# Kernel tuning notes

Hardware: AMD Instinct MI355X
Metric: run time of the kernel (lower is better)

Reference implementation:

```python
import jax, jax.numpy as jnp
import numpy as np

N, L, D = 4, 2048, 1024
H_DIM, OUT_DIM = 1024, 1024


def setup_inputs() -> dict:
    key = jax.random.key(0)
    ks = jax.random.split(key, 7)
    scale = 0.02
    return {
        "x": jax.random.normal(ks[0], (N, L, D), dtype=jnp.float32),
        "Wq": jax.random.normal(ks[1], (D, H_DIM), dtype=jnp.float32) * scale,
        "bq": jnp.zeros((H_DIM,), dtype=jnp.float32),
        "Wk": jax.random.normal(ks[2], (D, H_DIM), dtype=jnp.float32) * scale,
        "bk": jnp.zeros((H_DIM,), dtype=jnp.float32),
        "Wv": jax.random.normal(ks[3], (D, OUT_DIM), dtype=jnp.float32) * scale,
        "bv": jnp.zeros((OUT_DIM,), dtype=jnp.float32),
    }


def reference(x, Wq, bq, Wk, bk, Wv, bv):
    # q,k: [N,L,h_dim], v: [N,L,out_dim]
    q = jnp.einsum("nld,dh->nlh", x, Wq) + bq
    k = jnp.einsum("nld,dh->nlh", x, Wk) + bk
    v = jnp.einsum("nld,do->nlo", x, Wv) + bv
    # scores: [N,L,L]
    qk = jnp.einsum("nlh,nmh->nlm", q, k)
    # NOTE: original scales by sqrt(qk.shape[-1]) == sqrt(L) (seq len), not sqrt(h_dim)
    seq_len = qk.shape[-1]
    s = jax.nn.softmax(qk / jnp.sqrt(jnp.asarray(seq_len, dtype=qk.dtype)), axis=-1)
    return jnp.einsum("nlm,nmo->nlo", s, v)
```

## Files before the change

kernel.cpp:

```cpp
#include <hip/hip_runtime.h>
#include <hip/hip_bf16.h>


typedef __attribute__((ext_vector_type(8))) short bf16x8;
typedef __attribute__((ext_vector_type(4))) float f32x4;

#define AS_G(p) ((__attribute__((address_space(1))) void*)(p))
#define AS_L(p) ((__attribute__((address_space(3))) void*)(p))

__device__ __forceinline__ unsigned short f2bf(float f) {
  unsigned int u = __float_as_uint(f);
  unsigned int lsb = (u >> 16) & 1u;
  u += 0x7fffu + lsb;
  return (unsigned short)(u >> 16);
}

#define WAITV(n) asm volatile("s_waitcnt vmcnt(" #n ")" ::: "memory")
#define BAR() do { asm volatile("" ::: "memory");                             \
    __builtin_amdgcn_s_barrier();                                             \
    asm volatile("" ::: "memory"); } while (0)


#define BUFE 16384

#define S32A(ktk, rb, bofs)                                                   \
  __builtin_amdgcn_global_load_lds(                                           \
      AS_G(A + (size_t)(rowBase + (rb) * 32 + r0) * lda + (ktk) + goff),      \
      AS_L(lds + (bofs) + (rb) * 2048 + t * 8), 16, 0, 0)

#define S32B(ktk, rb, bofs)                                                   \
  __builtin_amdgcn_global_load_lds(                                           \
      AS_G(B + (size_t)(colBase + (rb) * 32 + r0) * ldb + (ktk) + goff),      \
      AS_L(lds + (bofs) + 8192 + (rb) * 2048 + t * 8), 16, 0, 0)

#define LDA4(bofs) do { _Pragma("unroll")                                     \
    for (int ks_ = 0; ks_ < 2; ks_++) { _Pragma("unroll")                     \
      for (int ii = 0; ii < 4; ii++) {                                        \
        int row_ = wrow + ii * 16 + r16;                                      \
        int slot_ = (ks_ * 4 + q) ^ (r16 & 7);                                \
        af[ks_][ii] = *(const bf16x8*)(lds + (bofs) + row_ * 64 + slot_ * 8); \
      } } } while (0)

#define LDB(jh, bofs) do { _Pragma("unroll")                                  \
    for (int ks_ = 0; ks_ < 2; ks_++) { _Pragma("unroll")                     \
      for (int jj = 0; jj < 2; jj++) {                                        \
        int row_ = wcol + ((jh) * 2 + jj) * 16 + r16;                         \
        int slot_ = (ks_ * 4 + q) ^ (r16 & 7);                                \
        bfr[ks_][(jh) * 2 + jj] =                                             \
            *(const bf16x8*)(lds + (bofs) + 8192 + row_ * 64 + slot_ * 8);    \
      } } } while (0)

#define MMQ(j0, j1) do { __builtin_amdgcn_s_setprio(1); _Pragma("unroll")     \
    for (int ks_ = 0; ks_ < 2; ks_++) { _Pragma("unroll")                     \
      for (int ii = 0; ii < 4; ii++) { _Pragma("unroll")                      \
        for (int jj = (j0); jj <= (j1); jj++)                                 \
          acc[ii][jj] = __builtin_amdgcn_mfma_f32_16x16x32_bf16(              \
              af[ks_][ii], bfr[ks_][jj], acc[ii][jj], 0, 0, 0);               \
      } }                                                                     \
    __builtin_amdgcn_s_setprio(0); } while (0)

#define TILE(ktc, bofs, obofs) do {                                           \
                      \
    LDA4(bofs); LDB(0, bofs);                                                 \
    if ((ktc) && (ktc) + 64 < K) {                                            \
      S32B((ktc) + 64, 0, obofs); S32B((ktc) + 64, 1, obofs);                 \
      S32B((ktc) + 64, 2, obofs); S32B((ktc) + 64, 3, obofs);                 \
    }                                                                         \
    BAR(); MMQ(0, 1); BAR();                                                  \
                  \
    LDB(1, bofs);                                                             \
    if ((ktc) + 128 < K) {                                                    \
      S32A((ktc) + 128, 0, bofs); S32A((ktc) + 128, 1, bofs);                 \
      S32A((ktc) + 128, 2, bofs); S32A((ktc) + 128, 3, bofs);                 \
    }                                                                         \
    BAR(); MMQ(2, 3);                                                         \
    if ((ktc) + 128 < K) { WAITV(4); } else { WAITV(0); }                     \
    BAR(); } while (0)

template <int EPI>
__global__ __launch_bounds__(256, 2) void gemm_db(
    const unsigned short* __restrict__ A, const unsigned short* __restrict__ B,
    float* __restrict__ Cf, long long sA, long long sB, long long sC,
    int K, int lda, int ldb, int ldc,
    unsigned short* __restrict__ u0, unsigned short* __restrict__ u1,
    unsigned short* __restrict__ u2,
    const float* __restrict__ f0, const float* __restrict__ f1,
    const float* __restrict__ f2,
    float* __restrict__ rsum, float scale)
{
  __shared__ unsigned short lds[2 * BUFE];

  const int t = threadIdx.x;
  const int rowBase = blockIdx.y * 128;
  const int colBase = blockIdx.x * 128;
  A += (long long)blockIdx.z * sA;
  B += (long long)blockIdx.z * sB;

  const int l = t & 63;
  const int w = t >> 6;
  const int wrow = (w >> 1) * 64;
  const int wcol = (w & 1) * 64;
  const int q = l >> 4;
  const int r16 = l & 15;

  const int r0 = t >> 3;
  const int goff = ((t & 7) ^ (r0 & 7)) << 3;

  f32x4 acc[4][4] = {};
  bf16x8 af[2][4], bfr[2][4];

  S32A(0, 0, 0); S32A(0, 1, 0); S32A(0, 2, 0); S32A(0, 3, 0);
  S32B(0, 0, 0); S32B(0, 1, 0); S32B(0, 2, 0); S32B(0, 3, 0);
  S32A(64, 0, BUFE); S32A(64, 1, BUFE); S32A(64, 2, BUFE); S32A(64, 3, BUFE);
  S32B(64, 0, BUFE); S32B(64, 1, BUFE); S32B(64, 2, BUFE); S32B(64, 3, BUFE);
  WAITV(8);
  BAR();

  for (int kt = 0; kt < K; kt += 128) {
    TILE(kt, 0, BUFE);
    TILE(kt + 64, BUFE, 0);
  }

  if (EPI == 1) {
    unsigned short* p16 = u0 + (long long)blockIdx.z * sC;
    float* rs = rsum + (long long)blockIdx.z * 2048;
#pragma unroll
    for (int i = 0; i < 4; i++) {
#pragma unroll
      for (int r = 0; r < 4; r++) {
        int row = rowBase + wrow + i * 16 + q * 4 + r;
        float rowpart = 0.f;
#pragma unroll
        for (int j = 0; j < 4; j++) {
          int col = colBase + wcol + j * 16 + r16;
          float e = __expf(acc[i][j][r] * scale);
          p16[(size_t)row * ldc + col] = f2bf(e);
          rowpart += e;
        }
#pragma unroll
        for (int m = 1; m < 16; m <<= 1) rowpart += __shfl_xor(rowpart, m);
        if (r16 == 0) atomicAdd(rs + row, rowpart);
      }
    }
  } else if (EPI == 2) {
    const int seg = colBase >> 10;
    if (seg < 2) {
      unsigned short* dst = seg ? u1 : u0;
      const float* bias = seg ? f1 : f0;
      const int cb = colBase & 1023;
#pragma unroll
      for (int i = 0; i < 4; i++) {
#pragma unroll
        for (int r = 0; r < 4; r++) {
          int row = rowBase + wrow + i * 16 + q * 4 + r;
#pragma unroll
          for (int j = 0; j < 4; j++) {
            int col = cb + wcol + j * 16 + r16;
            dst[(size_t)row * 1024 + col] = f2bf(acc[i][j][r] + bias[col]);
          }
        }
      }
    } else {
      const int ob = colBase - 2048;
#pragma unroll
      for (int i = 0; i < 4; i++) {
        int posBase = rowBase + wrow + i * 16 + q * 4;
        int b = posBase >> 11;
        int pos = posBase & 2047;
#pragma unroll
        for (int j = 0; j < 4; j++) {
          int o = ob + wcol + j * 16 + r16;
          float bias = f2[o];
          ushort4 pk;
          pk.x = f2bf(acc[i][j][0] + bias);
          pk.y = f2bf(acc[i][j][1] + bias);
          pk.z = f2bf(acc[i][j][2] + bias);
          pk.w = f2bf(acc[i][j][3] + bias);
          *(ushort4*)(u2 + ((size_t)((b << 10) + o) * 2048 + pos)) = pk;
        }
      }
    }
  } else {
    float* C = Cf + (long long)blockIdx.z * sC;
    const float* rs = rsum + (long long)blockIdx.z * 2048;
#pragma unroll
    for (int i = 0; i < 4; i++) {
#pragma unroll
      for (int r = 0; r < 4; r++) {
        int row = rowBase + wrow + i * 16 + q * 4 + r;
        float inv = 1.0f / rs[row];
#pragma unroll
        for (int j = 0; j < 4; j++) {
          int col = colBase + wcol + j * 16 + r16;
          C[(size_t)row * ldc + col] = acc[i][j][r] * inv;
        }
      }
    }
  }
}


__global__ __launch_bounds__(256) void cast_f32_to_bf16(
    const float* __restrict__ in, unsigned short* __restrict__ out, int n4,
    float* __restrict__ rzero, int nz4)
{
  int i = blockIdx.x * 256 + threadIdx.x;
  if (i < nz4) ((float4*)rzero)[i] = make_float4(0.f, 0.f, 0.f, 0.f);
  if (i >= n4) return;
  float4 v = ((const float4*)in)[i];
  ushort4 o;
  o.x = f2bf(v.x); o.y = f2bf(v.y); o.z = f2bf(v.z); o.w = f2bf(v.w);
  ((ushort4*)out)[i] = o;
}


__global__ __launch_bounds__(256) void wtrans(
    const float* __restrict__ Wq, const float* __restrict__ Wk,
    const float* __restrict__ Wv, unsigned short* __restrict__ WT)
{
  __shared__ float tile[32][33];
  const float* in = blockIdx.z == 0 ? Wq : (blockIdx.z == 1 ? Wk : Wv);
  unsigned short* out = WT + (size_t)blockIdx.z * 1024 * 1024;
  const int bc = blockIdx.x * 32;
  const int br = blockIdx.y * 32;
  const int tx = threadIdx.x;
  const int ty = threadIdx.y;
#pragma unroll
  for (int i = 0; i < 4; i++)
    tile[ty + i * 8][tx] = in[(size_t)(br + ty + i * 8) * 1024 + bc + tx];
  __syncthreads();
#pragma unroll
  for (int i = 0; i < 4; i++)
    out[(size_t)(bc + ty + i * 8) * 1024 + br + tx] = f2bf(tile[tx][ty + i * 8]);
}


extern "C" void kernel_launch(void* const* d_in, const int* in_sizes, int n_in,
                              void* d_out, int out_size, void* d_ws, size_t ws_size,
                              hipStream_t stream) {
  (void)in_sizes; (void)n_in; (void)out_size;

  const float* x  = (const float*)d_in[0];
  const float* Wq = (const float*)d_in[1];
  const float* bq = (const float*)d_in[2];
  const float* Wk = (const float*)d_in[3];
  const float* bk = (const float*)d_in[4];
  const float* Wv = (const float*)d_in[5];
  const float* bv = (const float*)d_in[6];
  float* out = (float*)d_out;

  const int Nb = 4, L = 2048, D = 1024, H = 1024, O = 1024;
  const int M = Nb * L;
  const int NQKV = 3 * H;

  char* ws = (char*)d_ws;
  size_t off = 0;
  unsigned short* xb = (unsigned short*)(ws + off); off += (size_t)M * D * 2;
  unsigned short* qb = (unsigned short*)(ws + off); off += (size_t)M * H * 2;
  unsigned short* kb = (unsigned short*)(ws + off); off += (size_t)M * H * 2;
  unsigned short* vt = (unsigned short*)(ws + off); off += (size_t)M * O * 2;
  unsigned short* WT = (unsigned short*)(ws + off); off += (size_t)NQKV * D * 2;
  unsigned short* P  = (unsigned short*)(ws + off); off += (size_t)Nb * L * L * 2;
  float* rsum = (float*)(ws + off); off += (size_t)Nb * L * 4;
  if (ws_size < off) return;

  dim3 blk256(256);

  cast_f32_to_bf16<<<(M * D / 4 + 255) / 256, blk256, 0, stream>>>(
      x, xb, M * D / 4, rsum, Nb * L / 4);

  wtrans<<<dim3(32, 32, 3), dim3(32, 8), 0, stream>>>(Wq, Wk, Wv, WT);

  gemm_db<2><<<dim3(NQKV / 128, M / 128, 1), blk256, 0, stream>>>(
      xb, WT, nullptr, 0, 0, 0, D, D, D, 0,
      qb, kb, vt, bq, bk, bv, nullptr, 0.f);

  gemm_db<1><<<dim3(L / 128, L / 128, Nb), blk256, 0, stream>>>(
      qb, kb, nullptr, (long long)L * H, (long long)L * H, (long long)L * L,
      H, H, H, L,
      P, nullptr, nullptr, nullptr, nullptr, nullptr,
      rsum, 0.022097086912079608f );

  gemm_db<3><<<dim3(O / 128, L / 128, Nb), blk256, 0, stream>>>(
      P, vt, out, (long long)L * L, (long long)O * L, (long long)L * O,
      L, L, L, O,
      nullptr, nullptr, nullptr, nullptr, nullptr, nullptr,
      rsum, 0.f);
}
```

Measured before the change: 240.5 us.

## Remap GEMM blocks with XCD-aware swizzle and merge prep kernels

The GEMM kernels now use a 1D grid and remap each block id so that consecutive tiles go to the same XCD (block id mod 8 grouping). Neighbouring tiles then share that XCD's L2 cache and reuse A/B panels. The separate cast and weight-transpose kernels are merged into one prep launch to remove a kernel launch. The remap assumes the grid size is divisible by 8 and adds integer division and modulo per block.

```diff
diff --git a/kernel.cpp b/kernel.cpp
--- a/kernel.cpp
+++ b/kernel.cpp
@@ -86,15 +86,23 @@
     unsigned short* __restrict__ u2,
     const float* __restrict__ f0, const float* __restrict__ f1,
     const float* __restrict__ f2,
-    float* __restrict__ rsum, float scale)
+    float* __restrict__ rsum, float scale, int gx, int gy)
 {
   __shared__ unsigned short lds[2 * BUFE];
 
   const int t = threadIdx.x;
-  const int rowBase = blockIdx.y * 128;
-  const int colBase = blockIdx.x * 128;
-  A += (long long)blockIdx.z * sA;
-  B += (long long)blockIdx.z * sB;
+
+  const int cpx = gridDim.x >> 3;
+  const int swz = (blockIdx.x & 7) * cpx + (blockIdx.x >> 3);
+  const int bx = swz % gx;
+  const int byz = swz / gx;
+  const int by = byz % gy;
+  const int bz = byz / gy;
+
+  const int rowBase = by * 128;
+  const int colBase = bx * 128;
+  A += (long long)bz * sA;
+  B += (long long)bz * sB;
 
   const int l = t & 63;
   const int w = t >> 6;
@@ -122,8 +130,8 @@
   }
 
   if (EPI == 1) {
-    unsigned short* p16 = u0 + (long long)blockIdx.z * sC;
-    float* rs = rsum + (long long)blockIdx.z * 2048;
+    unsigned short* p16 = u0 + (long long)bz * sC;
+    float* rs = rsum + (long long)bz * 2048;
 #pragma unroll
     for (int i = 0; i < 4; i++) {
 #pragma unroll
@@ -181,8 +189,8 @@
       }
     }
   } else {
-    float* C = Cf + (long long)blockIdx.z * sC;
-    const float* rs = rsum + (long long)blockIdx.z * 2048;
+    float* C = Cf + (long long)bz * sC;
+    const float* rs = rsum + (long long)bz * 2048;
 #pragma unroll
     for (int i = 0; i < 4; i++) {
 #pragma unroll
@@ -200,38 +208,41 @@
 }
 
 
-__global__ __launch_bounds__(256) void cast_f32_to_bf16(
-    const float* __restrict__ in, unsigned short* __restrict__ out, int n4,
-    float* __restrict__ rzero, int nz4)
-{
-  int i = blockIdx.x * 256 + threadIdx.x;
-  if (i < nz4) ((float4*)rzero)[i] = make_float4(0.f, 0.f, 0.f, 0.f);
-  if (i >= n4) return;
-  float4 v = ((const float4*)in)[i];
-  ushort4 o;
-  o.x = f2bf(v.x); o.y = f2bf(v.y); o.z = f2bf(v.z); o.w = f2bf(v.w);
-  ((ushort4*)out)[i] = o;
-}
-
-
-__global__ __launch_bounds__(256) void wtrans(
+__global__ __launch_bounds__(256) void prep(
+    const float* __restrict__ in, unsigned short* __restrict__ out,
+    float* __restrict__ rzero, int nz4,
     const float* __restrict__ Wq, const float* __restrict__ Wk,
     const float* __restrict__ Wv, unsigned short* __restrict__ WT)
 {
   __shared__ float tile[32][33];
-  const float* in = blockIdx.z == 0 ? Wq : (blockIdx.z == 1 ? Wk : Wv);
-  unsigned short* out = WT + (size_t)blockIdx.z * 1024 * 1024;
-  const int bc = blockIdx.x * 32;
-  const int br = blockIdx.y * 32;
-  const int tx = threadIdx.x;
-  const int ty = threadIdx.y;
-#pragma unroll
-  for (int i = 0; i < 4; i++)
-    tile[ty + i * 8][tx] = in[(size_t)(br + ty + i * 8) * 1024 + bc + tx];
-  __syncthreads();
-#pragma unroll
-  for (int i = 0; i < 4; i++)
-    out[(size_t)(bc + ty + i * 8) * 1024 + br + tx] = f2bf(tile[tx][ty + i * 8]);
+  const int bid = blockIdx.x;
+  const int t = threadIdx.x;
+  if (bid < 8192) {
+    int i = bid * 256 + t;
+    if (i < nz4) ((float4*)rzero)[i] = make_float4(0.f, 0.f, 0.f, 0.f);
+    float4 v = ((const float4*)in)[i];
+    ushort4 o;
+    o.x = f2bf(v.x); o.y = f2bf(v.y); o.z = f2bf(v.z); o.w = f2bf(v.w);
+    ((ushort4*)out)[i] = o;
+  } else {
+    const int b = bid - 8192;
+    const int z = b >> 10;
+    const int by = (b & 1023) >> 5;
+    const int bx = b & 31;
+    const float* src = z == 0 ? Wq : (z == 1 ? Wk : Wv);
+    unsigned short* dst = WT + (size_t)z * 1024 * 1024;
+    const int bc = bx * 32;
+    const int br = by * 32;
+    const int tx = t & 31;
+    const int ty = t >> 5;
+#pragma unroll
+    for (int i = 0; i < 4; i++)
+      tile[ty + i * 8][tx] = src[(size_t)(br + ty + i * 8) * 1024 + bc + tx];
+    __syncthreads();
+#pragma unroll
+    for (int i = 0; i < 4; i++)
+      dst[(size_t)(bc + ty + i * 8) * 1024 + br + tx] = f2bf(tile[tx][ty + i * 8]);
+  }
 }
 
 
@@ -266,24 +277,22 @@
 
   dim3 blk256(256);
 
-  cast_f32_to_bf16<<<(M * D / 4 + 255) / 256, blk256, 0, stream>>>(
-      x, xb, M * D / 4, rsum, Nb * L / 4);
-
-  wtrans<<<dim3(32, 32, 3), dim3(32, 8), 0, stream>>>(Wq, Wk, Wv, WT);
-
-  gemm_db<2><<<dim3(NQKV / 128, M / 128, 1), blk256, 0, stream>>>(
+  prep<<<dim3(8192 + 3072), blk256, 0, stream>>>(
+      x, xb, rsum, Nb * L / 4, Wq, Wk, Wv, WT);
+
+  gemm_db<2><<<dim3(1536), blk256, 0, stream>>>(
       xb, WT, nullptr, 0, 0, 0, D, D, D, 0,
-      qb, kb, vt, bq, bk, bv, nullptr, 0.f);
-
-  gemm_db<1><<<dim3(L / 128, L / 128, Nb), blk256, 0, stream>>>(
+      qb, kb, vt, bq, bk, bv, nullptr, 0.f, 24, 64);
+
+  gemm_db<1><<<dim3(1024), blk256, 0, stream>>>(
       qb, kb, nullptr, (long long)L * H, (long long)L * H, (long long)L * L,
       H, H, H, L,
       P, nullptr, nullptr, nullptr, nullptr, nullptr,
-      rsum, 0.022097086912079608f );
-
-  gemm_db<3><<<dim3(O / 128, L / 128, Nb), blk256, 0, stream>>>(
+      rsum, 0.022097086912079608f , 16, 16);
+
+  gemm_db<3><<<dim3(512), blk256, 0, stream>>>(
       P, vt, out, (long long)L * L, (long long)O * L, (long long)L * O,
       L, L, L, O,
       nullptr, nullptr, nullptr, nullptr, nullptr, nullptr,
-      rsum, 0.f);
-}
+      rsum, 0.f, 8, 16);
+}
```

New measurement: 221.9 us. -7.7%, faster.
